# Kernel optimization log

Hardware: AMD Instinct MI355X
Metric: run time of the kernel (lower is better)

The kernel has to match this reference:

```python
import jax, jax.numpy as jnp
import numpy as np

DIM, HEADS, DH, M, PINV_ITERS, RES_K = 512, 8, 64, 256, 6, 33

def layernorm(x, w, b, eps=1e-5):
    mu = jnp.mean(x, -1, keepdims=True)
    var = jnp.var(x, -1, keepdims=True)
    return (x - mu) * jax.lax.rsqrt(var + eps) * w + b

def pinv_iter(x, iters=PINV_ITERS):
    # Moore-Penrose iterative pseudo-inverse (lucidrains nystrom-attention)
    ax = jnp.abs(x)
    z = jnp.swapaxes(x, -1, -2) / (jnp.max(ax.sum(-1)) * jnp.max(ax.sum(-2)))
    I = jnp.eye(x.shape[-1], dtype=x.dtype)
    for _ in range(iters):
        xz = x @ z
        z = 0.25 * z @ (13 * I - xz @ (15 * I - xz @ (7 * I - xz)))
    return z

def _core(x, w_qkv):
    b, n, _ = x.shape
    pad = (M - n % M) % M            # Nystrom pads at the FRONT to a multiple of m=256
    xp = jnp.pad(x, ((0, 0), (pad, 0), (0, 0)))
    npad = n + pad
    q, k, v = jnp.split(xp @ w_qkv, 3, axis=-1)
    split_heads = lambda t: t.reshape(b, npad, HEADS, DH).transpose(0, 2, 1, 3)
    q = split_heads(q) * (DH ** -0.5)
    k, v = split_heads(k), split_heads(v)
    l = npad // M                    # tokens per landmark
    q_l = q.reshape(b, HEADS, M, l, DH).mean(3)
    k_l = k.reshape(b, HEADS, M, l, DH).mean(3)
    return q, k, v, q_l, k_l, pad, n

def nystrom_out(x, w_qkv, w_out, b_out, res_kernel):
    q, k, v, q_l, k_l, pad, n = _core(x, w_qkv)
    attn1 = jax.nn.softmax(jnp.einsum('bhid,bhjd->bhij', q, k_l), -1)    # (b,h,N,M)
    attn2 = jax.nn.softmax(jnp.einsum('bhid,bhjd->bhij', q_l, k_l), -1)  # (b,h,M,M)
    attn3 = jax.nn.softmax(jnp.einsum('bhid,bhjd->bhij', q_l, k), -1)    # (b,h,M,N)
    out = (attn1 @ pinv_iter(attn2)) @ (attn3 @ v)
    # depthwise residual conv over sequence dim, per head
    out = out + jax.lax.conv_general_dilated(
        v, res_kernel, (1, 1), [(RES_K // 2, RES_K // 2), (0, 0)],
        dimension_numbers=('NCHW', 'OIHW', 'NCHW'), feature_group_count=HEADS)
    b = out.shape[0]
    out = out.transpose(0, 2, 1, 3).reshape(b, -1, HEADS * DH) @ w_out + b_out
    return out[:, -n:]

def nystrom_cls_row(x, w_qkv):
    # cls-token (query index pad, head 0) row of attn1 @ pinv(attn2) @ attn3;
    # identical math to the full (n x n) matrix row the torch code slices out.
    q, k, v, q_l, k_l, pad, n = _core(x, w_qkv)
    q0, k0, ql0, kl0 = q[:, 0], k[:, 0], q_l[:, 0], k_l[:, 0]
    attn2 = jax.nn.softmax(ql0 @ jnp.swapaxes(kl0, -1, -2), -1)   # (b,M,M)
    attn3 = jax.nn.softmax(ql0 @ jnp.swapaxes(k0, -1, -2), -1)    # (b,M,N)
    row1 = jax.nn.softmax(jnp.einsum('bd,bjd->bj', q0[:, pad], kl0), -1)
    row = jnp.einsum('bj,bjk->bk', row1, pinv_iter(attn2))
    row = jnp.einsum('bk,bkn->bn', row, attn3)                    # (b, N_padded)
    return row, pad

def dwconv(x, k, b, p):
    y = jax.lax.conv_general_dilated(x, k, (1, 1), [(p, p), (p, p)],
        dimension_numbers=('NCHW', 'OIHW', 'NCHW'), feature_group_count=x.shape[1])
    return y + b[None, :, None, None]

def leff(x, k7, b7, k5, b5, k3, b3, Hs, Ws):
    cls_t, feat = x[:, :1], x[:, 1:]
    B, N, C = feat.shape
    img = feat.transpose(0, 2, 1).reshape(B, C, Hs, Ws)
    y = dwconv(img, k7, b7, 3) + img + dwconv(img, k5, b5, 2) + dwconv(img, k3, b3, 1)
    y = y.reshape(B, C, Hs * Ws).transpose(0, 2, 1)
    return jnp.concatenate([cls_t, y], axis=1)

def setup_inputs():
    key = jax.random.key(0)
    ks = iter(jax.random.split(key, 32))
    n, n_classes = 22500, 2
    p = {}
    p['h'] = jax.random.normal(next(ks), (n, 1024), jnp.float32)
    p['fc1_w'] = jax.random.normal(next(ks), (1024, DIM), jnp.float32) * 0.02
    p['fc1_b'] = jnp.zeros((DIM,), jnp.float32)
    p['cls_token'] = jax.random.normal(next(ks), (1, 1, DIM), jnp.float32)
    for pre in ('l1', 'l2'):
        p[pre + '_ln_w'] = jnp.ones((DIM,), jnp.float32)
        p[pre + '_ln_b'] = jnp.zeros((DIM,), jnp.float32)
        p[pre + '_wqkv'] = jax.random.normal(next(ks), (DIM, 3 * HEADS * DH), jnp.float32) * 0.02
        p[pre + '_wout'] = jax.random.normal(next(ks), (HEADS * DH, DIM), jnp.float32) * 0.02
        p[pre + '_bout'] = jnp.zeros((DIM,), jnp.float32)
        p[pre + '_resk'] = jax.random.normal(next(ks), (HEADS, 1, RES_K, 1), jnp.float32) * 0.05
    for kk in (7, 5, 3):
        p['leff_k%d' % kk] = jax.random.normal(next(ks), (DIM, 1, kk, kk), jnp.float32) * 0.05
        p['leff_b%d' % kk] = jnp.zeros((DIM,), jnp.float32)
    p['norm_w'] = jnp.ones((DIM,), jnp.float32)
    p['norm_b'] = jnp.zeros((DIM,), jnp.float32)
    p['fc2_w'] = jax.random.normal(next(ks), (DIM, n_classes), jnp.float32) * 0.02
    p['fc2_b'] = jnp.zeros((n_classes,), jnp.float32)
    return p

def reference(h, fc1_w, fc1_b, cls_token,
              l1_ln_w, l1_ln_b, l1_wqkv, l1_wout, l1_bout, l1_resk,
              leff_k7, leff_b7, leff_k5, leff_b5, leff_k3, leff_b3,
              l2_ln_w, l2_ln_b, l2_wqkv, l2_wout, l2_bout, l2_resk,
              norm_w, norm_b, fc2_w, fc2_b):
    x = h[None]                                   # (1, n, 1024)
    n = x.shape[1]
    x = jax.nn.relu(x @ fc1_w + fc1_b)            # (1, n, 512)
    Hs = int(np.ceil(np.sqrt(n)))                 # 150 for n=22500
    add_len = Hs * Hs - n
    if add_len > 0:
        x = jnp.concatenate([x, x[:, :add_len]], axis=1)
    x = jnp.concatenate([jnp.broadcast_to(cls_token, (1, 1, DIM)), x], axis=1)
    # TransLayer 1
    x = x + nystrom_out(layernorm(x, l1_ln_w, l1_ln_b), l1_wqkv, l1_wout, l1_bout, l1_resk)
    # LeFF positional layer
    x = leff(x, leff_k7, leff_b7, leff_k5, leff_b5, leff_k3, leff_b3, Hs, Hs)
    # TransLayer 2 (first call in TransMIL.forward)
    h2 = x + nystrom_out(layernorm(x, l2_ln_w, l2_ln_b), l2_wqkv, l2_wout, l2_bout, l2_resk)
    # TransLayer 2 second call: residual update then attention matrix of updated state
    h3 = h2 + nystrom_out(layernorm(h2, l2_ln_w, l2_ln_b), l2_wqkv, l2_wout, l2_bout, l2_resk)
    row, pad = nystrom_cls_row(layernorm(h3, l2_ln_w, l2_ln_b), l2_wqkv)
    A = row[0, pad + 1: pad + 1 + n][:, None]     # (n, 1) cls->instance attention
    hf = layernorm(h2, norm_w, norm_b)[:, 0]      # (1, 512)
    logits = hf @ fc2_w + fc2_b                   # (1, n_classes)
    Y_prob = jax.nn.softmax(logits, -1)
    return logits, Y_prob, A
```

## Files before the change

### kernel.cpp

```cpp
#include <hip/hip_runtime.h>

#define NTOK 22500
#define N1   22501
#define NPAD 22528
#define PADR 27
#define DIM  512
#define NH   8
#define DHD  64
#define MM   256
#define LLM  88
#define HSZ  150
#define CSZ  256
#define NCH  88

typedef short bf16x8 __attribute__((ext_vector_type(8)));
typedef float f32x4  __attribute__((ext_vector_type(4)));
typedef unsigned short us;

union U8 { bf16x8 v; unsigned short u[8]; };

__device__ __forceinline__ unsigned short f2b(float f){
  unsigned int u = __float_as_uint(f);
  unsigned int r = u + 0x7fffu + ((u>>16)&1u);
  return (unsigned short)(r>>16);
}
__device__ __forceinline__ float bf2f(unsigned short u){
  return __uint_as_float(((unsigned int)u)<<16);
}
__device__ __forceinline__ bf16x8 cvt8(float4 a, float4 b){
  U8 u;
  u.u[0]=f2b(a.x); u.u[1]=f2b(a.y); u.u[2]=f2b(a.z); u.u[3]=f2b(a.w);
  u.u[4]=f2b(b.x); u.u[5]=f2b(b.y); u.u[6]=f2b(b.z); u.u[7]=f2b(b.w);
  return u.v;
}

__device__ __forceinline__ float waveSum(float v){
#pragma unroll
  for (int o=32;o>0;o>>=1) v += __shfl_down(v,o);
  return v;
}
__device__ __forceinline__ float waveMax(float v){
#pragma unroll
  for (int o=32;o>0;o>>=1) v = fmaxf(v,__shfl_down(v,o));
  return v;
}
__device__ __forceinline__ float blockSum256(float v, float* sb){
  v = waveSum(v);
  __syncthreads();
  if ((threadIdx.x&63)==0) sb[threadIdx.x>>6]=v;
  __syncthreads();
  return sb[0]+sb[1]+sb[2]+sb[3];
}
__device__ __forceinline__ float blockMax256(float v, float* sb){
  v = waveMax(v);
  __syncthreads();
  if ((threadIdx.x&63)==0) sb[threadIdx.x>>6]=v;
  __syncthreads();
  return fmaxf(fmaxf(sb[0],sb[1]),fmaxf(sb[2],sb[3]));
}

__global__ void k_wT(const float* __restrict__ W, us* __restrict__ Bt, int K, int N)
{
  __shared__ float tile[32][33];
  int tx = threadIdx.x&31, ty = threadIdx.x>>5;
  int k0 = blockIdx.x*32, n0 = blockIdx.y*32;
#pragma unroll
  for (int i=0;i<4;++i){
    int k = k0+ty+i*8;
    if (k<K && n0+tx<N) tile[ty+i*8][tx] = W[(size_t)k*N + n0+tx];
  }
  __syncthreads();
#pragma unroll
  for (int i=0;i<4;++i){
    int n = n0+ty+i*8, k = k0+tx;
    if (n<N && k<K) Bt[(size_t)n*K + k] = f2b(tile[tx][ty+i*8]);
  }
}

__global__ void k_vT(const us* __restrict__ V, us* __restrict__ Vt)
{
  __shared__ us tile[32][33];
  int tx = threadIdx.x&31, ty = threadIdx.x>>5;
  int p0 = blockIdx.x*32;
  int h = blockIdx.y>>1, d0 = (blockIdx.y&1)*32;
#pragma unroll
  for (int i=0;i<4;++i){
    int p = p0+ty+i*8;
    tile[ty+i*8][tx] = V[((size_t)h*NPAD+p)*DHD + d0+tx];
  }
  __syncthreads();
#pragma unroll
  for (int i=0;i<4;++i){
    int d = d0+ty+i*8;
    Vt[((size_t)h*DHD+d)*NPAD + p0+tx] = tile[tx][ty+i*8];
  }
}

template<int MODE>
__global__ __launch_bounds__(256) void k_gemm(const float* __restrict__ Af,
    const us* __restrict__ Ab, const us* __restrict__ Bt, const float* __restrict__ bias,
    float* __restrict__ Cf, float* __restrict__ C2,
    us* __restrict__ Q_, us* __restrict__ K_, us* __restrict__ V_, int Kd)
{
  __shared__ us SM[16384];
  us* As = SM;
  us* Bs = SM + 8192;
  const int tid = threadIdx.x;
  const int m0 = blockIdx.x*128, n0 = blockIdx.y*128;
  const int lane = tid & 63;
  const int wid = tid >> 6;
  const int wm = (wid>>1)*64, wn = (wid&1)*64;
  f32x4 acc[4][4] = {};
  for (int k0=0; k0<Kd; k0+=64){
    __syncthreads();
#pragma unroll
    for (int i=0;i<8;++i){
      int g = i*256 + tid;
      int row = g>>4, k4 = (g&15)*4;
      int gm = m0 + row;
      ushort4 h4 = make_ushort4(0,0,0,0);
      if (MODE==0){
        if (gm < NTOK){
          float4 v = *(const float4*)(Af + (size_t)gm*Kd + k0 + k4);
          h4.x=f2b(v.x); h4.y=f2b(v.y); h4.z=f2b(v.z); h4.w=f2b(v.w);
        }
      } else if (MODE==1 || MODE==3){
        if (gm >= PADR) h4 = *(const ushort4*)(Ab + (size_t)(gm-PADR)*Kd + k0 + k4);
      } else {
        if (gm < N1) h4 = *(const ushort4*)(Ab + (size_t)(gm+PADR)*Kd + k0 + k4);
      }
      *(ushort4*)(&As[row*64 + (k4 ^ ((row&7)<<3))]) = h4;
    }
#pragma unroll
    for (int i=0;i<8;++i){
      int g = i*256 + tid;
      int col = g>>4, k4 = (g&15)*4;
      int vn = n0 + col;
      if (MODE==3) vn = (vn<64) ? vn : vn+448;
      ushort4 h4 = *(const ushort4*)(Bt + (size_t)vn*Kd + k0 + k4);
      *(ushort4*)(&Bs[col*64 + (k4 ^ ((col&7)<<3))]) = h4;
    }
    __syncthreads();
#pragma unroll
    for (int ks=0; ks<2; ++ks){
      const int kk = ks*32 + (lane>>4)*8;
      bf16x8 af[4], bfm[4];
#pragma unroll
      for (int t=0;t<4;++t){
        int r = wm + t*16 + (lane&15);
        af[t] = *(bf16x8*)(&As[r*64 + (kk ^ ((r&7)<<3))]);
        int c = wn + t*16 + (lane&15);
        bfm[t] = *(bf16x8*)(&Bs[c*64 + (kk ^ ((c&7)<<3))]);
      }
#pragma unroll
      for (int mt=0;mt<4;++mt)
#pragma unroll
        for (int nt=0;nt<4;++nt)
          acc[mt][nt] = __builtin_amdgcn_mfma_f32_16x16x32_bf16(af[mt], bfm[nt], acc[mt][nt], 0,0,0);
    }
  }
  const int rbase = (lane>>4)*4;
  const int cl = lane&15;
  if (MODE==1){
    const int sec = blockIdx.y>>2;
    const float sc = sec==0 ? 0.125f : 1.f;
    __syncthreads();
#pragma unroll
    for (int mt=0;mt<4;++mt)
#pragma unroll
      for (int r=0;r<4;++r){
        int row = wm + mt*16 + rbase + r;
#pragma unroll
        for (int nt=0;nt<4;++nt){
          int col = wn + nt*16 + cl;
          SM[row*128 + col] = f2b(acc[mt][nt][r]*sc);
        }
      }
    __syncthreads();
    us* dst = sec==0 ? Q_ : (sec==1 ? K_ : V_);
#pragma unroll
    for (int i=0;i<8;++i){
      int v8 = i*256 + tid;
      int row = v8>>4, c8 = (v8&15)*8;
      int gm = m0 + row, gn = n0 + c8;
      int hh = (gn>>6)&7, d = gn&63;
      *(bf16x8*)(dst + ((size_t)hh*NPAD+gm)*DHD + d) = *(bf16x8*)(&SM[row*128 + c8]);
    }
  } else {
#pragma unroll
    for (int mt=0;mt<4;++mt){
#pragma unroll
      for (int r=0;r<4;++r){
        int gm = m0 + wm + mt*16 + rbase + r;
#pragma unroll
        for (int nt=0;nt<4;++nt){
          int gn = n0 + wn + nt*16 + cl;
          float v = acc[mt][nt][r];
          if (MODE==0){
            if (gm < NTOK){ float o = v + bias[gn]; Cf[(size_t)(1+gm)*DIM + gn] = o>0.f?o:0.f; }
          } else if (MODE==2){
            if (gm < N1) Cf[(size_t)gm*DIM + gn] += v + bias[gn];
          } else {
            if (gn < 64) Cf[(size_t)gm*DHD + gn] = v*0.125f;
            else         C2[(size_t)gm*DHD + (gn-64)] = v;
          }
        }
      }
    }
  }
}

__global__ void k_setcls(float* __restrict__ X, const float* __restrict__ cls){
  int i = blockIdx.x*256 + threadIdx.x;
  if (i < DIM) X[i] = cls[i];
}
__global__ void k_copy(float* __restrict__ d, const float* __restrict__ s, size_t n){
  size_t i = (size_t)blockIdx.x*256 + threadIdx.x;
  if (i<n) d[i]=s[i];
}

__global__ void k_ln(const float* __restrict__ X, us* __restrict__ Y,
                     const float* __restrict__ w, const float* __restrict__ b)
{
  __shared__ float sb[4];
  const float* x = X + (size_t)blockIdx.x*DIM;
  us* y = Y + (size_t)blockIdx.x*DIM;
  int t = threadIdx.x;
  float a0=x[t], a1=x[t+256];
  float s = blockSum256(a0+a1, sb);
  float q = blockSum256(a0*a0+a1*a1, sb);
  float mean = s*(1.f/512.f);
  float var = q*(1.f/512.f) - mean*mean;
  float rstd = rsqrtf(var+1e-5f);
  y[t]     = f2b((a0-mean)*rstd*w[t]+b[t]);
  y[t+256] = f2b((a1-mean)*rstd*w[t+256]+b[t+256]);
}

__global__ void k_landmark_b(const us* __restrict__ src, us* __restrict__ dst)
{
  int hm = blockIdx.x; int h = hm>>8, m = hm&255; int d = threadIdx.x;
  const us* base = src + ((size_t)h*NPAD + (size_t)m*LLM)*DHD + d;
  float s = 0.f;
  for (int j=0;j<LLM;++j) s += bf2f(base[(size_t)j*DHD]);
  dst[((size_t)h*MM + m)*DHD + d] = f2b(s * (1.f/(float)LLM));
}
__global__ void k_landmark(const float* __restrict__ src, float* __restrict__ dst)
{
  int hm = blockIdx.x; int h = hm>>8, m = hm&255; int d = threadIdx.x;
  const float* base = src + ((size_t)h*NPAD + (size_t)m*LLM)*DHD + d;
  float s = 0.f;
  for (int j=0;j<LLM;++j) s += base[(size_t)j*DHD];
  dst[((size_t)h*MM + m)*DHD + d] = s * (1.f/(float)LLM);
}

__global__ __launch_bounds__(64) void k_nt64(const float* __restrict__ A,
    const float* __restrict__ B, float* __restrict__ C,
    long sA, long sB, long sC, int Nr)
{
  int lane = threadIdx.x;
  int n0 = blockIdx.x*64, m0 = blockIdx.y*64;
  A += (size_t)blockIdx.z*sA; B += (size_t)blockIdx.z*sB; C += (size_t)blockIdx.z*sC;
  f32x4 acc[4][4] = {};
#pragma unroll
  for (int ks=0;ks<2;++ks){
    int kk = ks*32 + (lane>>4)*8;
    bf16x8 af[4], bfr[4];
#pragma unroll
    for (int mt=0;mt<4;++mt){
      const float* p = A + (size_t)(m0+mt*16+(lane&15))*64 + kk;
      af[mt] = cvt8(*(const float4*)p, *(const float4*)(p+4));
    }
#pragma unroll
    for (int nt=0;nt<4;++nt){
      const float* p = B + (size_t)(n0+nt*16+(lane&15))*64 + kk;
      bfr[nt] = cvt8(*(const float4*)p, *(const float4*)(p+4));
    }
#pragma unroll
    for (int mt=0;mt<4;++mt)
#pragma unroll
      for (int nt=0;nt<4;++nt)
        acc[mt][nt] = __builtin_amdgcn_mfma_f32_16x16x32_bf16(af[mt], bfr[nt], acc[mt][nt], 0,0,0);
  }
#pragma unroll
  for (int mt=0;mt<4;++mt)
#pragma unroll
    for (int r=0;r<4;++r){
      int row = m0+mt*16+(lane>>4)*4+r;
#pragma unroll
      for (int nt=0;nt<4;++nt){
        int col = n0+nt*16+(lane&15);
        C[(size_t)row*Nr + col] = acc[mt][nt][r];
      }
    }
}

__global__ __launch_bounds__(64) void k_nt64b(const us* __restrict__ A,
    const us* __restrict__ B, float* __restrict__ C,
    long sA, long sB, long sC, int Nr)
{
  int lane = threadIdx.x;
  int n0 = blockIdx.x*64, m0 = blockIdx.y*64;
  A += (size_t)blockIdx.z*sA; B += (size_t)blockIdx.z*sB; C += (size_t)blockIdx.z*sC;
  f32x4 acc[4][4] = {};
#pragma unroll
  for (int ks=0;ks<2;++ks){
// ... 43 lines not shown
  __syncthreads();
  const int wm = (wid>>1)*32, wn = (wid&1)*32;
  f32x4 acc[2][2] = {};
#pragma unroll
  for (int ks=0;ks<8;++ks){
    int kk = ks*32 + (lane>>4)*8;
    bf16x8 af[2], bfr[2];
#pragma unroll
    for (int t=0;t<2;++t){
      int rr = wm + t*16 + (lane&15);
      af[t] = *(const bf16x8*)(&As[rr*256 + (kk ^ ((rr&7)<<3))]);
      int cc = wn + t*16 + (lane&15);
      bfr[t] = *(const bf16x8*)(&Bs[cc*256 + (kk ^ ((cc&7)<<3))]);
    }
#pragma unroll
    for (int mt=0;mt<2;++mt)
#pragma unroll
      for (int nt=0;nt<2;++nt)
        acc[mt][nt] = __builtin_amdgcn_mfma_f32_16x16x32_bf16(af[mt], bfr[nt], acc[mt][nt], 0,0,0);
  }
#pragma unroll
  for (int mt=0;mt<2;++mt)
#pragma unroll
    for (int r=0;r<4;++r){
      int row = m0 + wm + mt*16 + (lane>>4)*4 + r;
#pragma unroll
      for (int nt=0;nt<2;++nt){
        int col = n0 + wn + nt*16 + (lane&15);
        float v = acc[mt][nt][r];
        if (PM==1) v = alpha*(dc*bf2f(Ab[(size_t)row*256+col]) - v);
        if (PM==2){
          Ct[(size_t)blockIdx.z*16384 + (size_t)col*256 + row] = f2b(v);
        } else {
          us bv = f2b(v);
          if (PM==0 || writeC) C[(size_t)blockIdx.z*65536 + (size_t)row*256 + col] = bv;
          Ct[(size_t)blockIdx.z*65536 + (size_t)col*256 + row] = bv;
        }
      }
    }
}

__global__ void k_softmax256(float* __restrict__ S, us* __restrict__ Sb)
{
  __shared__ float sb[4];
  float* row = S + ((size_t)blockIdx.x<<8);
  float x = row[threadIdx.x];
  float m = blockMax256(x, sb);
  float e = __expf(x-m);
  float s = blockSum256(e, sb);
  float p = e/s;
  row[threadIdx.x] = p;
  Sb[((size_t)blockIdx.x<<8) + threadIdx.x] = f2b(p);
}
__global__ void k_rcsum(const float* __restrict__ A2, float* __restrict__ sums, int nb)
{
  __shared__ float sb[4];
  int b = blockIdx.x >> 8, r = blockIdx.x & 255;
  const float* Ab = A2 + ((size_t)b<<16);
  float v = (blockIdx.y==0) ? Ab[((size_t)r<<8) + threadIdx.x]
                            : Ab[((size_t)threadIdx.x<<8) + r];
  float s = blockSum256(v, sb);
  if (threadIdx.x==0) sums[(size_t)blockIdx.y*nb + blockIdx.x] = s;
}
__global__ void k_scale(const float* __restrict__ sums, float* __restrict__ scl, int nb)
{
  __shared__ float sb[4];
  float mr=-1e30f, mc=-1e30f;
  for (int i=threadIdx.x;i<nb;i+=256) mr = fmaxf(mr, sums[i]);
  for (int i=threadIdx.x;i<nb;i+=256) mc = fmaxf(mc, sums[nb+i]);
  mr = blockMax256(mr, sb);
  mc = blockMax256(mc, sb);
  if (threadIdx.x==0) scl[0] = 1.f/(mr*mc);
}
__global__ void k_z0(const float* __restrict__ A2, us* __restrict__ Z, us* __restrict__ Zt,
                     const float* __restrict__ scl)
{
  size_t idx = (size_t)blockIdx.x*256 + threadIdx.x;
  size_t b = idx>>16; int i=(int)((idx>>8)&255), j=(int)(idx&255);
  float v = A2[idx]*scl[0];
  us bv = f2b(v);
  Zt[idx] = bv;
  Z[(b<<16)+((size_t)j<<8)+i] = bv;
}

__global__ __launch_bounds__(256) void k_attn3(const us* __restrict__ QLb,
    const us* __restrict__ Kb, const us* __restrict__ Vt,
    float* __restrict__ Pmax, float* __restrict__ Psum, us* __restrict__ Pacc)
{
  __shared__ us Ks[64*64];
  __shared__ us Vs[64*64];
  __shared__ us Ps[4*64*64];
  int h = blockIdx.y, cx = blockIdx.x;
  int tid = threadIdx.x, wid = tid>>6, lane = tid&63;
  bf16x8 aq[4][2];
#pragma unroll
  for (int mt=0;mt<4;++mt){
    const us* qp = QLb + ((size_t)h*MM + wid*64 + mt*16 + (lane&15))*DHD;
#pragma unroll
    for (int ks=0;ks<2;++ks)
      aq[mt][ks] = *(const bf16x8*)(qp + ks*32 + (lane>>4)*8);
  }
  float m_[4][4], l_[4][4];
  f32x4 acc[4][4] = {};
#pragma unroll
  for (int mt=0;mt<4;++mt)
#pragma unroll
    for (int r=0;r<4;++r){ m_[mt][r] = -1e30f; l_[mt][r] = 0.f; }

  us* Pw = &Ps[wid*4096];
  for (int t=0;t<4;++t){
    int kb0 = cx*CSZ + t*64;
    __syncthreads();
    for (int i=tid;i<1024;i+=256){
      int rr = i>>4, c4 = (i&15)*4;
      ushort4 ku = *(const ushort4*)(Kb + ((size_t)h*NPAD + kb0 + rr)*DHD + c4);
      *(ushort4*)(&Ks[rr*64 + (c4 ^ ((rr&7)<<3))]) = ku;
      ushort4 vu = *(const ushort4*)(Vt + ((size_t)h*DHD + rr)*NPAD + kb0 + c4);
      *(ushort4*)(&Vs[rr*64 + (c4 ^ ((rr&7)<<3))]) = vu;
    }
    __syncthreads();
    f32x4 s[4][4] = {};
#pragma unroll
    for (int ks=0;ks<2;++ks){
      int kk = ks*32 + (lane>>4)*8;
      bf16x8 kbf[4];
// ... 162 lines not shown
    int kk = ks*32 + (lane>>4)*8;
    bf16x8 a = *(const bf16x8*)(&Ps[arow*256 + (kk ^ ((arow&7)<<3))]);
#pragma unroll
    for (int dt=0;dt<4;++dt){
      int d = dt*16 + (lane&15);
      bf16x8 b = *(const bf16x8*)(&KWs[d*256 + (kk ^ ((d&7)<<3))]);
      acc[dt] = __builtin_amdgcn_mfma_f32_16x16x32_bf16(a, b, acc[dt], 0,0,0);
    }
  }
#pragma unroll
  for (int r=0;r<4;++r){
    int row = q0 + prow_base + r;
    us* op = OH + (size_t)row*DIM + h*DHD;
#pragma unroll
    for (int dt=0;dt<4;++dt)
      op[dt*16 + (lane&15)] = f2b(acc[dt][r]*rcp[r]);
  }
}

#define SCBLK 32
__global__ __launch_bounds__(256) void k_seqconv(const us* __restrict__ Vb,
    const float* __restrict__ resk, us* __restrict__ OH)
{
  __shared__ us Vs[64*512];
  int tid = threadIdx.x;
  int p0 = blockIdx.x*SCBLK;
  for (int i=tid; i<16384; i+=256){
    int pl = i>>8, c2 = i&255;
    int gp = p0 - 16 + pl;
    int hh = c2>>5, d2 = (c2&31)*2;
    ushort2 v = make_ushort2(0,0);
    if (gp>=0 && gp<NPAD) v = *(const ushort2*)(Vb + ((size_t)hh*NPAD+gp)*DHD + d2);
    *(ushort2*)(&Vs[pl*512 + c2*2]) = v;
  }
  __syncthreads();
  int h = tid>>5;
  float kr[33];
#pragma unroll
  for (int r=0;r<33;++r) kr[r] = resk[h*33+r];
  for (int pl=0; pl<SCBLK; ++pl){
    float s0=0.f, s1=0.f;
#pragma unroll
    for (int r=0;r<33;++r){
      ushort2 v = *(const ushort2*)(&Vs[(pl+r)*512 + tid*2]);
      s0 += bf2f(v.x)*kr[r];
      s1 += bf2f(v.y)*kr[r];
    }
    size_t o = (size_t)(p0+pl)*DIM + tid*2;
    ushort2 cur = *(ushort2*)(OH + o);
    *(ushort2*)(OH + o) = make_ushort2(f2b(bf2f(cur.x)+s0), f2b(bf2f(cur.y)+s1));
  }
}

__global__ void k_tfwd(const float* __restrict__ X, us* __restrict__ T)
{
  __shared__ float tile[32][33];
  int tx = threadIdx.x & 31, ty = threadIdx.x >> 5;
  int s0 = blockIdx.x*32, c0 = blockIdx.y*32;
  for (int yy=0; yy<4; ++yy){
    int s = s0 + ty + yy*8;
    if (s < NTOK) tile[ty+yy*8][tx] = X[(size_t)(1+s)*DIM + c0+tx];
  }
  __syncthreads();
  for (int yy=0; yy<4; ++yy){
    int c = c0 + ty + yy*8;
    int s = s0 + tx;
    if (s < NTOK) T[(size_t)c*NTOK + s] = f2b(tile[tx][ty+yy*8]);
  }
}
__global__ void k_tbwd(const us* __restrict__ T, float* __restrict__ X)
{
  __shared__ float tile[32][33];
  int tx = threadIdx.x & 31, ty = threadIdx.x >> 5;
  int s0 = blockIdx.x*32, c0 = blockIdx.y*32;
  for (int yy=0; yy<4; ++yy){
    int c = c0 + ty + yy*8, s = s0 + tx;
    if (s < NTOK) tile[ty+yy*8][tx] = bf2f(T[(size_t)c*NTOK + s]);
  }
  __syncthreads();
  for (int yy=0; yy<4; ++yy){
    int s = s0 + ty + yy*8, c = c0 + tx;
    if (s < NTOK) X[(size_t)(1+s)*DIM + c] = tile[tx][ty+yy*8];
  }
}
__global__ __launch_bounds__(256) void k_leff(const us* __restrict__ T,
    const float* __restrict__ k7, const float* __restrict__ b7,
    const float* __restrict__ k5, const float* __restrict__ b5,
    const float* __restrict__ k3, const float* __restrict__ b3,
    us* __restrict__ T2)
{
  __shared__ float tile[21*21];
  int c = blockIdx.y;
  int ti = blockIdx.x/10, tj = blockIdx.x%10;
  int i0 = ti*15-3, j0 = tj*15-3;
  const us* img = T + (size_t)c*NTOK;
  for (int idx=threadIdx.x; idx<441; idx+=256){
    int ii = idx/21, jj = idx%21;
    int gi = i0+ii, gj = j0+jj;
    tile[idx] = (gi>=0 && gi<HSZ && gj>=0 && gj<HSZ) ? bf2f(img[gi*HSZ+gj]) : 0.f;
  }
  __syncthreads();
  if (threadIdx.x < 225){
    int li = threadIdx.x/15, lj = threadIdx.x%15;
    int gi = ti*15+li, gj = tj*15+lj;
    float acc = tile[(li+3)*21 + (lj+3)] + b7[c]+b5[c]+b3[c];
    const float* w7 = k7 + c*49;
#pragma unroll
    for (int a=0;a<7;++a)
#pragma unroll
      for (int bb=0;bb<7;++bb) acc += tile[(li+a)*21 + (lj+bb)]*w7[a*7+bb];
    const float* w5 = k5 + c*25;
#pragma unroll
    for (int a=0;a<5;++a)
#pragma unroll
      for (int bb=0;bb<5;++bb) acc += tile[(li+1+a)*21 + (lj+1+bb)]*w5[a*5+bb];
    const float* w3 = k3 + c*9;
#pragma unroll
    for (int a=0;a<3;++a)
#pragma unroll
      for (int bb=0;bb<3;++bb) acc += tile[(li+2+a)*21 + (lj+2+bb)]*w3[a*3+bb];
    T2[(size_t)c*NTOK + gi*HSZ+gj] = f2b(acc);
  }
}

__global__ void k_row1(const float* __restrict__ Q0, const float* __restrict__ KL0,
                       float* __restrict__ row1)
{
  __shared__ float sb[4];
  __shared__ float qv[64];
  int t = threadIdx.x;
  if (t<64) qv[t] = Q0[PADR*DHD + t];
  __syncthreads();
  float l = 0.f;
#pragma unroll
  for (int d=0;d<64;++d) l += qv[d]*KL0[(size_t)t*DHD+d];
  float m = blockMax256(l, sb);
  float e = __expf(l-m);
  float s = blockSum256(e, sb);
  row1[t] = e/s;
}
__global__ void k_rz(const float* __restrict__ row1, const us* __restrict__ Zt,
                     float* __restrict__ rz)
{
  __shared__ float r1[256];
  int t = threadIdx.x;
  r1[t] = row1[t];
  __syncthreads();
  float s = 0.f;
  for (int k2=0;k2<256;++k2) s += r1[k2]*bf2f(Zt[(size_t)t*MM + k2]);
  rz[t] = s;
}
__global__ void k_rowstat(const float* __restrict__ L0, float* __restrict__ mx, float* __restrict__ se)
{
  __shared__ float sb[4];
  const float* row = L0 + (size_t)blockIdx.x*NPAD;
  float m = -1e30f;
  for (int i=threadIdx.x;i<NPAD;i+=256) m = fmaxf(m, row[i]);
  m = blockMax256(m, sb);
  float s = 0.f;
  for (int i=threadIdx.x;i<NPAD;i+=256) s += __expf(row[i]-m);
  s = blockSum256(s, sb);
  if (threadIdx.x==0){ mx[blockIdx.x]=m; se[blockIdx.x]=s; }
}
__global__ void k_aout(const float* __restrict__ L0, const float* __restrict__ rz,
    const float* __restrict__ mx, const float* __restrict__ se, float* __restrict__ out)
{
  __shared__ float wk[256], mk[256];
  int t = threadIdx.x;
  wk[t] = rz[t]/se[t];
  mk[t] = mx[t];
  __syncthreads();
  int p = blockIdx.x*256 + t;
  if (p >= NTOK) return;
  size_t pp = (size_t)(PADR+1+p);
  float a = 0.f;
  for (int k2=0;k2<256;++k2) a += wk[k2]*__expf(L0[(size_t)k2*NPAD+pp]-mk[k2]);
  out[4+p] = a;
}
__global__ void k_final(const float* __restrict__ H2r, const float* __restrict__ nw,
    const float* __restrict__ nbb, const float* __restrict__ w2, const float* __restrict__ b2,
    float* __restrict__ out)
{
  __shared__ float sb[4];
  __shared__ float hf[512];
  int t = threadIdx.x;
  float x0 = H2r[t], x1 = H2r[256+t];
  float s = blockSum256(x0+x1, sb);
  float q = blockSum256(x0*x0+x1*x1, sb);
  float mean = s*(1.f/512.f);
  float var = q*(1.f/512.f) - mean*mean;
  float rstd = rsqrtf(var+1e-5f);
  hf[t]     = (x0-mean)*rstd*nw[t]+nbb[t];
  hf[256+t] = (x1-mean)*rstd*nw[256+t]+nbb[256+t];
  __syncthreads();
  float p0 = hf[t]*w2[t*2]   + hf[256+t]*w2[(256+t)*2];
  float p1 = hf[t]*w2[t*2+1] + hf[256+t]*w2[(256+t)*2+1];
  p0 = blockSum256(p0, sb);
  p1 = blockSum256(p1, sb);
  if (t==0){
    float l0 = p0+b2[0], l1 = p1+b2[1];
    float m = fmaxf(l0,l1);
    float e0 = __expf(l0-m), e1 = __expf(l1-m), si = 1.f/(e0+e1);
    out[0]=l0; out[1]=l1; out[2]=e0*si; out[3]=e1*si;
  }
}

struct Bufs {
  float *X,*A2,*sums,*scl,*Pmax,*Psum;
  us *Yb,*OHb,*Qb,*Kb,*Vb,*Vtb,*QLb,*KLb,*A2b;
  us *Z0b,*Z0tb,*Z1b,*Z1tb,*XZb,*XZtb,*T1tb,*T2tb;
  us *A3Vtb,*WmT,*Pacc;
};

static void run_pinv(const us* A2b, Bufs& b, int NB, hipStream_t st,
                     us** outZ, us** outZt)
{
  dim3 g(4,4,NB);
  us *Zc=b.Z0b, *Zct=b.Z0tb, *Zn=b.Z1b, *Znt=b.Z1tb;
  for (int it=0; it<6; ++it){
    k_pgemm<0><<<g,256,0,st>>>(A2b, Zct, b.XZb, b.XZtb, 0.f, 1.f, 1);
    k_pgemm<1><<<g,256,0,st>>>(b.XZb, b.XZtb, nullptr, b.T1tb, 7.f, 1.f, 0);
    k_pgemm<1><<<g,256,0,st>>>(b.XZb, b.T1tb, nullptr, b.T2tb, 15.f, 1.f, 0);
    k_pgemm<1><<<g,256,0,st>>>(Zc, b.T2tb, Zn, Znt, 13.f, 0.25f, 1);
    us* t1=Zc; Zc=Zn; Zn=t1;
    us* t2=Zct; Zct=Znt; Znt=t2;
  }
  *outZ = Zc; *outZt = Zct;
}

static void nystrom_layer(Bufs& b, const float* lnw, const float* lnb,
    const us* wqkvT, const us* woutT,
    const float* bout, const float* resk, hipStream_t st)
{
  k_ln<<<N1,256,0,st>>>(b.X, b.Yb, lnw, lnb);
  k_gemm<1><<<dim3(NPAD/128,12),256,0,st>>>(nullptr, b.Yb, wqkvT, nullptr,
      nullptr, nullptr, b.Qb, b.Kb, b.Vb, DIM);
  k_vT<<<dim3(NPAD/32,16),256,0,st>>>(b.Vb, b.Vtb);
  k_landmark_b<<<NH*MM,64,0,st>>>(b.Qb, b.QLb);
  k_landmark_b<<<NH*MM,64,0,st>>>(b.Kb, b.KLb);
  k_nt64b<<<dim3(4,4,NH),64,0,st>>>(b.QLb, b.KLb, b.A2,
      (long)MM*DHD,(long)MM*DHD,(long)MM*MM, MM);
  k_softmax256<<<NH*MM,256,0,st>>>(b.A2, b.A2b);
  k_rcsum<<<dim3(NH*MM,2),256,0,st>>>(b.A2, b.sums, NH*MM);
  k_scale<<<1,256,0,st>>>(b.sums, b.scl, NH*MM);
  k_z0<<<NH*MM*MM/256,256,0,st>>>(b.A2, b.Z0b, b.Z0tb, b.scl);
  us *Zc, *Zct;
  run_pinv(b.A2b, b, NH, st, &Zc, &Zct);
  k_attn3<<<dim3(NCH,NH),256,0,st>>>(b.QLb, b.Kb, b.Vtb, b.Pmax, b.Psum, b.Pacc);
  k_attn3_merge<<<NH*MM,64,0,st>>>(b.Pmax, b.Psum, b.Pacc, b.A3Vtb);
  k_pgemm<2><<<dim3(1,4,NH),256,0,st>>>(Zc, b.A3Vtb, nullptr, b.WmT, 0.f, 1.f, 0);
  k_attn1<<<dim3(NPAD/64,NH),256,0,st>>>(b.Qb, b.KLb, b.WmT, b.OHb);
  k_seqconv<<<NPAD/SCBLK,256,0,st>>>(b.Vb, resk, b.OHb);
  k_gemm<2><<<dim3(176,4),256,0,st>>>(nullptr, b.OHb, woutT, bout,
      b.X, nullptr, nullptr, nullptr, nullptr, DIM);
}

extern "C" void kernel_launch(void* const* d_in, const int* in_sizes, int n_in,
                              void* d_out, int out_size, void* d_ws, size_t ws_size,
                              hipStream_t stream)
{
  (void)n_in; (void)out_size;
  bool sig_order = (in_sizes[10] == 25088);
  int iL2 = sig_order ? 16 : 10;
  int iLf = sig_order ? 10 : 16;

  const float* h       = (const float*)d_in[0];
  const float* fc1_w   = (const float*)d_in[1];
  const float* fc1_b   = (const float*)d_in[2];
  const float* cls_tok = (const float*)d_in[3];
  const float* l1_lnw  = (const float*)d_in[4];
  const float* l1_lnb  = (const float*)d_in[5];
  const float* l1_wqkv = (const float*)d_in[6];
  const float* l1_wout = (const float*)d_in[7];
  const float* l1_bout = (const float*)d_in[8];
  const float* l1_resk = (const float*)d_in[9];
  const float* l2_lnw  = (const float*)d_in[iL2+0];
  const float* l2_lnb  = (const float*)d_in[iL2+1];
  const float* l2_wqkv = (const float*)d_in[iL2+2];
  const float* l2_wout = (const float*)d_in[iL2+3];
  const float* l2_bout = (const float*)d_in[iL2+4];
  const float* l2_resk = (const float*)d_in[iL2+5];
  const float* k7 = (const float*)d_in[iLf+0];
  const float* b7 = (const float*)d_in[iLf+1];
  const float* k5 = (const float*)d_in[iLf+2];
  const float* b5 = (const float*)d_in[iLf+3];
  const float* k3 = (const float*)d_in[iLf+4];
  const float* b3 = (const float*)d_in[iLf+5];
  const float* nw = (const float*)d_in[22];
  const float* nbb= (const float*)d_in[23];
  const float* w2 = (const float*)d_in[24];
  const float* b2 = (const float*)d_in[25];
  float* out = (float*)d_out;

  char* base = (char*)d_ws;
  auto allocF = [&](size_t n)->float*{
    float* p=(float*)base; base += ((n*sizeof(float)+255)&~(size_t)255); return p; };
  auto allocU = [&](size_t n)->us*{
    us* p=(us*)base; base += ((n*sizeof(us)+255)&~(size_t)255); return p; };

  const size_t S = (size_t)NPAD*DIM;
  const size_t SQ = (size_t)MM*MM;
  Bufs b;
  b.X   = allocF(S);
  b.Yb  = allocU(S);
  b.OHb = allocU(S);
  b.Qb  = allocU(S);
  b.Kb  = allocU(S);
  b.Vb  = allocU(S);
  b.Vtb = allocU(S);
  b.QLb = allocU((size_t)NH*MM*DHD);
  b.KLb = allocU((size_t)NH*MM*DHD);
  b.A2  = allocF((size_t)NH*SQ);
  b.A2b = allocU((size_t)NH*SQ);
  b.Z0b = allocU((size_t)NH*SQ);  b.Z0tb = allocU((size_t)NH*SQ);
  b.Z1b = allocU((size_t)NH*SQ);  b.Z1tb = allocU((size_t)NH*SQ);
  b.XZb = allocU((size_t)NH*SQ);  b.XZtb = allocU((size_t)NH*SQ);
  b.T1tb= allocU((size_t)NH*SQ);
  b.T2tb= allocU((size_t)NH*SQ);
  b.A3Vtb = allocU((size_t)NH*MM*DHD);
  b.WmT   = allocU((size_t)NH*MM*DHD);
  b.sums  = allocF(2*(size_t)NH*MM);
  b.scl   = allocF(16);
  b.Pmax  = allocF((size_t)NH*NCH*MM);
  b.Psum  = allocF((size_t)NH*NCH*MM);
  b.Pacc  = allocU((size_t)NH*NCH*MM*DHD);
  us* fc1T   = allocU((size_t)DIM*1024);
  us* wqkvT1 = allocU((size_t)1536*DIM);
  us* wqkvT2 = allocU((size_t)1536*DIM);
  us* woutT1 = allocU((size_t)DIM*DIM);
  us* woutT2 = allocU((size_t)DIM*DIM);
  float* Q0   = allocF((size_t)NPAD*DHD);
  float* K0   = allocF((size_t)NPAD*DHD);
  float* QL0f = allocF((size_t)MM*DHD);
  float* KL0f = allocF((size_t)MM*DHD);
  float* row1 = allocF(256);
  float* rzv  = allocF(256);
  float* mxv  = allocF(256);
  float* sev  = allocF(256);
  float* h2row= allocF(512);
  if ((size_t)(base - (char*)d_ws) > ws_size) return;

  k_wT<<<dim3(32,16),256,0,stream>>>(fc1_w, fc1T, 1024, DIM);
  k_wT<<<dim3(16,48),256,0,stream>>>(l1_wqkv, wqkvT1, DIM, 1536);
  k_wT<<<dim3(16,48),256,0,stream>>>(l2_wqkv, wqkvT2, DIM, 1536);
  k_wT<<<dim3(16,16),256,0,stream>>>(l1_wout, woutT1, DIM, DIM);
  k_wT<<<dim3(16,16),256,0,stream>>>(l2_wout, woutT2, DIM, DIM);

  k_gemm<0><<<dim3(176,4),256,0,stream>>>(h, nullptr, fc1T, fc1_b,
      b.X, nullptr, nullptr, nullptr, nullptr, 1024);
  k_setcls<<<2,256,0,stream>>>(b.X, cls_tok);

  nystrom_layer(b, l1_lnw, l1_lnb, wqkvT1, woutT1, l1_bout, l1_resk, stream);
  k_tfwd<<<dim3(704,16),256,0,stream>>>(b.X, b.OHb);
  k_leff<<<dim3(100,512),256,0,stream>>>(b.OHb, k7,b7,k5,b5,k3,b3, b.Qb);
  k_tbwd<<<dim3(704,16),256,0,stream>>>(b.Qb, b.X);

  nystrom_layer(b, l2_lnw, l2_lnb, wqkvT2, woutT2, l2_bout, l2_resk, stream);
  k_copy<<<2,256,0,stream>>>(h2row, b.X, 512);

  nystrom_layer(b, l2_lnw, l2_lnb, wqkvT2, woutT2, l2_bout, l2_resk, stream);

  k_ln<<<N1,256,0,stream>>>(b.X, b.Yb, l2_lnw, l2_lnb);
  k_gemm<3><<<dim3(176,1),256,0,stream>>>(nullptr, b.Yb, wqkvT2, nullptr,
      Q0, K0, nullptr, nullptr, nullptr, DIM);
  k_landmark<<<MM,64,0,stream>>>(Q0, QL0f);
  k_landmark<<<MM,64,0,stream>>>(K0, KL0f);
  k_nt64<<<dim3(4,4,1),64,0,stream>>>(QL0f, KL0f, b.A2, 0,0,0, MM);
  k_softmax256<<<MM,256,0,stream>>>(b.A2, b.A2b);
  k_rcsum<<<dim3(MM,2),256,0,stream>>>(b.A2, b.sums, MM);
  k_scale<<<1,256,0,stream>>>(b.sums, b.scl, MM);
  k_z0<<<MM*MM/256,256,0,stream>>>(b.A2, b.Z0b, b.Z0tb, b.scl);
  us *Zc, *Zct;
  run_pinv(b.A2b, b, 1, stream, &Zc, &Zct);
  k_row1<<<1,256,0,stream>>>(Q0, KL0f, row1);
  k_rz<<<1,256,0,stream>>>(row1, Zct, rzv);
  float* L0 = (float*)b.Yb;
  k_nt64<<<dim3(NPAD/64,4,1),64,0,stream>>>(QL0f, K0, L0, 0,0,0, NPAD);
  k_rowstat<<<MM,256,0,stream>>>(L0, mxv, sev);
  k_aout<<<88,256,0,stream>>>(L0, rzv, mxv, sev, out);
  k_final<<<1,256,0,stream>>>(h2row, nw, nbb, w2, b2, out);
}
```

Measured before the change: 2.640 ms.

## Store residual stream in bf16, use direct global-to-LDS loads, merge small kernels

The residual activation buffer changes from fp32 to bf16, which halves traffic in layernorm, the output-projection residual add, the transposes and the fc1 epilogue. GEMM operand staging now uses global_load_lds 16-byte direct loads with a zero page for padded rows, and epilogues go through LDS for vectorized bf16 stores. Landmark kernels are merged, and the row/column-sum scale is replaced by a per-matrix column-sum max using the softmax row-sum-equals-one property. Rounding the residual to bf16 on every layer adds precision risk.

Result: faster. 2.487 ms (-5.8%).

```diff
diff --git a/kernel.cpp b/kernel.cpp
--- a/kernel.cpp
+++ b/kernel.cpp
@@ -33,6 +33,11 @@
   u.u[4]=f2b(b.x); u.u[5]=f2b(b.y); u.u[6]=f2b(b.z); u.u[7]=f2b(b.w);
   return u.v;
 }
+__device__ __forceinline__ void gld16(const void* g, void* l){
+  __builtin_amdgcn_global_load_lds(
+      (const __attribute__((address_space(1))) void*)g,
+      (__attribute__((address_space(3))) void*)l, 16, 0, 0);
+}
 
 __device__ __forceinline__ float waveSum(float v){
 #pragma unroll
@@ -99,8 +104,9 @@
 template<int MODE>
 __global__ __launch_bounds__(256) void k_gemm(const float* __restrict__ Af,
     const us* __restrict__ Ab, const us* __restrict__ Bt, const float* __restrict__ bias,
-    float* __restrict__ Cf, float* __restrict__ C2,
-    us* __restrict__ Q_, us* __restrict__ K_, us* __restrict__ V_, int Kd)
+    us* __restrict__ Xb, float* __restrict__ Cf, float* __restrict__ C2,
+    us* __restrict__ Q_, us* __restrict__ K_, us* __restrict__ V_,
+    const us* __restrict__ zpg, int Kd)
 {
   __shared__ us SM[16384];
   us* As = SM;
@@ -113,32 +119,40 @@
   f32x4 acc[4][4] = {};
   for (int k0=0; k0<Kd; k0+=64){
     __syncthreads();
-#pragma unroll
-    for (int i=0;i<8;++i){
-      int g = i*256 + tid;
-      int row = g>>4, k4 = (g&15)*4;
-      int gm = m0 + row;
-      ushort4 h4 = make_ushort4(0,0,0,0);
-      if (MODE==0){
+    if (MODE==0){
+#pragma unroll
+      for (int i=0;i<8;++i){
+        int g = i*256 + tid;
+        int row = g>>4, k4 = (g&15)*4;
+        int gm = m0 + row;
+        ushort4 h4 = make_ushort4(0,0,0,0);
         if (gm < NTOK){
           float4 v = *(const float4*)(Af + (size_t)gm*Kd + k0 + k4);
           h4.x=f2b(v.x); h4.y=f2b(v.y); h4.z=f2b(v.z); h4.w=f2b(v.w);
         }
-      } else if (MODE==1 || MODE==3){
-        if (gm >= PADR) h4 = *(const ushort4*)(Ab + (size_t)(gm-PADR)*Kd + k0 + k4);
-      } else {
-        if (gm < N1) h4 = *(const ushort4*)(Ab + (size_t)(gm+PADR)*Kd + k0 + k4);
-      }
-      *(ushort4*)(&As[row*64 + (k4 ^ ((row&7)<<3))]) = h4;
-    }
-#pragma unroll
-    for (int i=0;i<8;++i){
-      int g = i*256 + tid;
-      int col = g>>4, k4 = (g&15)*4;
-      int vn = n0 + col;
-      if (MODE==3) vn = (vn<64) ? vn : vn+448;
-      ushort4 h4 = *(const ushort4*)(Bt + (size_t)vn*Kd + k0 + k4);
-      *(ushort4*)(&Bs[col*64 + (k4 ^ ((col&7)<<3))]) = h4;
+        *(ushort4*)(&As[row*64 + (k4 ^ ((row&7)<<3))]) = h4;
+      }
+    } else {
+#pragma unroll
+      for (int i=0;i<4;++i){
+        int c = wid*4+i;
+        int row = c*8 + (lane>>3);
+        int scol8 = ((lane&7) ^ (row&7))*8;
+        int gm = m0+row;
+        const us* ga;
+        if (MODE==2) ga = Ab + ((size_t)((gm<N1?gm:0)+PADR))*Kd + k0 + scol8;
+        else ga = (gm>=PADR) ? Ab + (size_t)(gm-PADR)*Kd + k0 + scol8 : zpg + scol8;
+        gld16(ga, &As[c*512]);
+      }
+    }
+#pragma unroll
+    for (int i=0;i<4;++i){
+      int c = wid*4+i;
+      int row = c*8 + (lane>>3);
+      int scol8 = ((lane&7) ^ (row&7))*8;
+      int vn = n0+row;
+      if (MODE==3) vn = (vn<64)? vn : vn+448;
+      gld16(Bt + (size_t)vn*Kd + k0 + scol8, &Bs[c*512]);
     }
     __syncthreads();
 #pragma unroll
@@ -161,22 +175,42 @@
   }
   const int rbase = (lane>>4)*4;
   const int cl = lane&15;
+  if (MODE==3){
+#pragma unroll
+    for (int mt=0;mt<4;++mt)
+#pragma unroll
+      for (int r=0;r<4;++r){
+        int gm = m0 + wm + mt*16 + rbase + r;
+#pragma unroll
+        for (int nt=0;nt<4;++nt){
+          int gn = n0 + wn + nt*16 + cl;
+          float v = acc[mt][nt][r];
+          if (gn < 64) Cf[(size_t)gm*DHD + gn] = v*0.125f;
+          else         C2[(size_t)gm*DHD + (gn-64)] = v;
+        }
+      }
+    return;
+  }
+  const float sc1 = (MODE==1 && (blockIdx.y>>2)==0) ? 0.125f : 1.f;
+  __syncthreads();
+#pragma unroll
+  for (int mt=0;mt<4;++mt)
+#pragma unroll
+    for (int r=0;r<4;++r){
+      int row = wm + mt*16 + rbase + r;
+#pragma unroll
+      for (int nt=0;nt<4;++nt){
+        int col = wn + nt*16 + cl;
+        float v = acc[mt][nt][r];
+        if (MODE==0){ v += bias[n0+col]; v = v>0.f?v:0.f; }
+        else if (MODE==2){ v += bias[n0+col]; }
+        else v *= sc1;
+        SM[row*128 + col] = f2b(v);
+      }
+    }
+  __syncthreads();
   if (MODE==1){
     const int sec = blockIdx.y>>2;
-    const float sc = sec==0 ? 0.125f : 1.f;
-    __syncthreads();
-#pragma unroll
-    for (int mt=0;mt<4;++mt)
-#pragma unroll
-      for (int r=0;r<4;++r){
-        int row = wm + mt*16 + rbase + r;
-#pragma unroll
-        for (int nt=0;nt<4;++nt){
-          int col = wn + nt*16 + cl;
-          SM[row*128 + col] = f2b(acc[mt][nt][r]*sc);
-        }
-      }
-    __syncthreads();
     us* dst = sec==0 ? Q_ : (sec==1 ? K_ : V_);
 #pragma unroll
     for (int i=0;i<8;++i){
@@ -186,71 +220,87 @@
       int hh = (gn>>6)&7, d = gn&63;
       *(bf16x8*)(dst + ((size_t)hh*NPAD+gm)*DHD + d) = *(bf16x8*)(&SM[row*128 + c8]);
     }
+  } else if (MODE==0){
+#pragma unroll
+    for (int i=0;i<8;++i){
+      int v8 = i*256 + tid;
+      int row = v8>>4, c8 = (v8&15)*8;
+      int gm = m0 + row;
+      if (gm < NTOK)
+        *(bf16x8*)(Xb + (size_t)(1+gm)*DIM + n0 + c8) = *(bf16x8*)(&SM[row*128 + c8]);
+    }
   } else {
 #pragma unroll
-    for (int mt=0;mt<4;++mt){
-#pragma unroll
-      for (int r=0;r<4;++r){
-        int gm = m0 + wm + mt*16 + rbase + r;
-#pragma unroll
-        for (int nt=0;nt<4;++nt){
-          int gn = n0 + wn + nt*16 + cl;
-          float v = acc[mt][nt][r];
-          if (MODE==0){
-            if (gm < NTOK){ float o = v + bias[gn]; Cf[(size_t)(1+gm)*DIM + gn] = o>0.f?o:0.f; }
-          } else if (MODE==2){
-            if (gm < N1) Cf[(size_t)gm*DIM + gn] += v + bias[gn];
-          } else {
-            if (gn < 64) Cf[(size_t)gm*DHD + gn] = v*0.125f;
-            else         C2[(size_t)gm*DHD + (gn-64)] = v;
-          }
-        }
-      }
-    }
-  }
-}
-
-__global__ void k_setcls(float* __restrict__ X, const float* __restrict__ cls){
+    for (int i=0;i<8;++i){
+      int v8 = i*256 + tid;
+      int row = v8>>4, c8 = (v8&15)*8;
+      int gm = m0 + row;
+      if (gm < N1){
+        us* p = Xb + (size_t)gm*DIM + n0 + c8;
+        U8 xo, ad, o;
+        xo.v = *(bf16x8*)p;
+        ad.v = *(bf16x8*)(&SM[row*128 + c8]);
+#pragma unroll
+        for (int j=0;j<8;++j) o.u[j] = f2b(bf2f(xo.u[j]) + bf2f(ad.u[j]));
+        *(bf16x8*)p = o.v;
+      }
+    }
+  }
+}
+
+__global__ void k_setcls(us* __restrict__ X, const float* __restrict__ cls){
   int i = blockIdx.x*256 + threadIdx.x;
-  if (i < DIM) X[i] = cls[i];
-}
-__global__ void k_copy(float* __restrict__ d, const float* __restrict__ s, size_t n){
+  if (i < DIM) X[i] = f2b(cls[i]);
+}
+__global__ void k_copyu(us* __restrict__ d, const us* __restrict__ s, size_t n){
   size_t i = (size_t)blockIdx.x*256 + threadIdx.x;
   if (i<n) d[i]=s[i];
 }
 
-__global__ void k_ln(const float* __restrict__ X, us* __restrict__ Y,
+__global__ void k_ln(const us* __restrict__ X, us* __restrict__ Y,
                      const float* __restrict__ w, const float* __restrict__ b)
 {
   __shared__ float sb[4];
-  const float* x = X + (size_t)blockIdx.x*DIM;
+  const us* x = X + (size_t)blockIdx.x*DIM;
   us* y = Y + (size_t)blockIdx.x*DIM;
   int t = threadIdx.x;
-  float a0=x[t], a1=x[t+256];
+  ushort2 xv = *(const ushort2*)(x + 2*t);
+  float a0=bf2f(xv.x), a1=bf2f(xv.y);
   float s = blockSum256(a0+a1, sb);
   float q = blockSum256(a0*a0+a1*a1, sb);
   float mean = s*(1.f/512.f);
   float var = q*(1.f/512.f) - mean*mean;
   float rstd = rsqrtf(var+1e-5f);
-  y[t]     = f2b((a0-mean)*rstd*w[t]+b[t]);
-  y[t+256] = f2b((a1-mean)*rstd*w[t+256]+b[t+256]);
-}
-
-__global__ void k_landmark_b(const us* __restrict__ src, us* __restrict__ dst)
-{
-  int hm = blockIdx.x; int h = hm>>8, m = hm&255; int d = threadIdx.x;
-  const us* base = src + ((size_t)h*NPAD + (size_t)m*LLM)*DHD + d;
+  float2 wv = *(const float2*)(w + 2*t);
+  float2 bv = *(const float2*)(b + 2*t);
+  ushort2 o;
+  o.x = f2b((a0-mean)*rstd*wv.x+bv.x);
+  o.y = f2b((a1-mean)*rstd*wv.y+bv.y);
+  *(ushort2*)(y + 2*t) = o;
+}
+
+__global__ void k_landmark2(const us* __restrict__ Q, const us* __restrict__ K,
+                            us* __restrict__ QL, us* __restrict__ KL)
+{
+  int hm = blockIdx.x;
+  bool isK = hm >= NH*MM;
+  if (isK) hm -= NH*MM;
+  int h = hm>>8, m = hm&255; int d = threadIdx.x;
+  const us* base = (isK?K:Q) + ((size_t)h*NPAD + (size_t)m*LLM)*DHD + d;
   float s = 0.f;
   for (int j=0;j<LLM;++j) s += bf2f(base[(size_t)j*DHD]);
-  dst[((size_t)h*MM + m)*DHD + d] = f2b(s * (1.f/(float)LLM));
-}
-__global__ void k_landmark(const float* __restrict__ src, float* __restrict__ dst)
-{
-  int hm = blockIdx.x; int h = hm>>8, m = hm&255; int d = threadIdx.x;
-  const float* base = src + ((size_t)h*NPAD + (size_t)m*LLM)*DHD + d;
+  (isK?KL:QL)[((size_t)h*MM + m)*DHD + d] = f2b(s * (1.f/(float)LLM));
+}
+__global__ void k_landmark2f(const float* __restrict__ Q, const float* __restrict__ K,
+                             float* __restrict__ QL, float* __restrict__ KL)
+{
+  int hm = blockIdx.x;
+  bool isK = hm >= MM;
+  int m = isK ? hm-MM : hm; int d = threadIdx.x;
+  const float* base = (isK?K:Q) + (size_t)m*LLM*DHD + d;
   float s = 0.f;
   for (int j=0;j<LLM;++j) s += base[(size_t)j*DHD];
-  dst[((size_t)h*MM + m)*DHD + d] = s * (1.f/(float)LLM);
+  (isK?KL:QL)[(size_t)m*DHD + d] = s * (1.f/(float)LLM);
 }
 
 __global__ __launch_bounds__(64) void k_nt64(const float* __restrict__ A,
@@ -400,25 +450,23 @@
   row[threadIdx.x] = p;
   Sb[((size_t)blockIdx.x<<8) + threadIdx.x] = f2b(p);
 }
-__global__ void k_rcsum(const float* __restrict__ A2, float* __restrict__ sums, int nb)
+__global__ void k_csmax(const float* __restrict__ A2, float* __restrict__ sums)
 {
   __shared__ float sb[4];
-  int b = blockIdx.x >> 8, r = blockIdx.x & 255;
+  int b = blockIdx.x, j = threadIdx.x;
   const float* Ab = A2 + ((size_t)b<<16);
-  float v = (blockIdx.y==0) ? Ab[((size_t)r<<8) + threadIdx.x]
-                            : Ab[((size_t)threadIdx.x<<8) + r];
-  float s = blockSum256(v, sb);
-  if (threadIdx.x==0) sums[(size_t)blockIdx.y*nb + blockIdx.x] = s;
-}
-__global__ void k_scale(const float* __restrict__ sums, float* __restrict__ scl, int nb)
+  float s = 0.f;
+  for (int i=0;i<256;++i) s += Ab[((size_t)i<<8)+j];
+  float m = blockMax256(s, sb);
+  if (j==0) sums[b] = m;
+}
+__global__ void k_scale2(const float* __restrict__ sums, float* __restrict__ scl, int nb)
 {
   __shared__ float sb[4];
-  float mr=-1e30f, mc=-1e30f;
-  for (int i=threadIdx.x;i<nb;i+=256) mr = fmaxf(mr, sums[i]);
-  for (int i=threadIdx.x;i<nb;i+=256) mc = fmaxf(mc, sums[nb+i]);
-  mr = blockMax256(mr, sb);
-  mc = blockMax256(mc, sb);
-  if (threadIdx.x==0) scl[0] = 1.f/(mr*mc);
+  float m=-1e30f;
+  for (int i=threadIdx.x;i<nb;i+=256) m = fmaxf(m, sums[i]);
+  m = blockMax256(m, sb);
+  if (threadIdx.x==0) scl[0] = 1.f/m;
 }
 __global__ void k_z0(const float* __restrict__ A2, us* __restrict__ Z, us* __restrict__ Zt,
                      const float* __restrict__ scl)
@@ -687,9 +735,9 @@
   }
 }
 
-__global__ void k_tfwd(const float* __restrict__ X, us* __restrict__ T)
-{
-  __shared__ float tile[32][33];
+__global__ void k_tfwd(const us* __restrict__ X, us* __restrict__ T)
+{
+  __shared__ us tile[32][33];
   int tx = threadIdx.x & 31, ty = threadIdx.x >> 5;
   int s0 = blockIdx.x*32, c0 = blockIdx.y*32;
   for (int yy=0; yy<4; ++yy){
@@ -700,17 +748,17 @@
   for (int yy=0; yy<4; ++yy){
     int c = c0 + ty + yy*8;
     int s = s0 + tx;
-    if (s < NTOK) T[(size_t)c*NTOK + s] = f2b(tile[tx][ty+yy*8]);
-  }
-}
-__global__ void k_tbwd(const us* __restrict__ T, float* __restrict__ X)
-{
-  __shared__ float tile[32][33];
+    if (s < NTOK) T[(size_t)c*NTOK + s] = tile[tx][ty+yy*8];
+  }
+}
+__global__ void k_tbwd(const us* __restrict__ T, us* __restrict__ X)
+{
+  __shared__ us tile[32][33];
   int tx = threadIdx.x & 31, ty = threadIdx.x >> 5;
   int s0 = blockIdx.x*32, c0 = blockIdx.y*32;
   for (int yy=0; yy<4; ++yy){
     int c = c0 + ty + yy*8, s = s0 + tx;
-    if (s < NTOK) tile[ty+yy*8][tx] = bf2f(T[(size_t)c*NTOK + s]);
+    if (s < NTOK) tile[ty+yy*8][tx] = T[(size_t)c*NTOK + s];
   }
   __syncthreads();
   for (int yy=0; yy<4; ++yy){
@@ -812,14 +860,14 @@
   for (int k2=0;k2<256;++k2) a += wk[k2]*__expf(L0[(size_t)k2*NPAD+pp]-mk[k2]);
   out[4+p] = a;
 }
-__global__ void k_final(const float* __restrict__ H2r, const float* __restrict__ nw,
+__global__ void k_final(const us* __restrict__ H2r, const float* __restrict__ nw,
     const float* __restrict__ nbb, const float* __restrict__ w2, const float* __restrict__ b2,
     float* __restrict__ out)
 {
   __shared__ float sb[4];
   __shared__ float hf[512];
   int t = threadIdx.x;
-  float x0 = H2r[t], x1 = H2r[256+t];
+  float x0 = bf2f(H2r[t]), x1 = bf2f(H2r[256+t]);
   float s = blockSum256(x0+x1, sb);
   float q = blockSum256(x0*x0+x1*x1, sb);
   float mean = s*(1.f/512.f);
@@ -841,10 +889,10 @@
 }
 
 struct Bufs {
-  float *X,*A2,*sums,*scl,*Pmax,*Psum;
-  us *Yb,*OHb,*Qb,*Kb,*Vb,*Vtb,*QLb,*KLb,*A2b;
+  float *A2,*sums,*scl,*Pmax,*Psum;
+  us *Xb,*Yb,*OHb,*Qb,*Kb,*Vb,*Vtb,*QLb,*KLb,*A2b;
   us *Z0b,*Z0tb,*Z1b,*Z1tb,*XZb,*XZtb,*T1tb,*T2tb;
-  us *A3Vtb,*WmT,*Pacc;
+  us *A3Vtb,*WmT,*Pacc,*zpg;
 };
 
 static void run_pinv(const us* A2b, Bufs& b, int NB, hipStream_t st,
@@ -867,17 +915,16 @@
     const us* wqkvT, const us* woutT,
     const float* bout, const float* resk, hipStream_t st)
 {
-  k_ln<<<N1,256,0,st>>>(b.X, b.Yb, lnw, lnb);
+  k_ln<<<N1,256,0,st>>>(b.Xb, b.Yb, lnw, lnb);
   k_gemm<1><<<dim3(NPAD/128,12),256,0,st>>>(nullptr, b.Yb, wqkvT, nullptr,
-      nullptr, nullptr, b.Qb, b.Kb, b.Vb, DIM);
+      nullptr, nullptr, nullptr, b.Qb, b.Kb, b.Vb, b.zpg, DIM);
   k_vT<<<dim3(NPAD/32,16),256,0,st>>>(b.Vb, b.Vtb);
-  k_landmark_b<<<NH*MM,64,0,st>>>(b.Qb, b.QLb);
-  k_landmark_b<<<NH*MM,64,0,st>>>(b.Kb, b.KLb);
+  k_landmark2<<<2*NH*MM,64,0,st>>>(b.Qb, b.Kb, b.QLb, b.KLb);
   k_nt64b<<<dim3(4,4,NH),64,0,st>>>(b.QLb, b.KLb, b.A2,
       (long)MM*DHD,(long)MM*DHD,(long)MM*MM, MM);
   k_softmax256<<<NH*MM,256,0,st>>>(b.A2, b.A2b);
-  k_rcsum<<<dim3(NH*MM,2),256,0,st>>>(b.A2, b.sums, NH*MM);
-  k_scale<<<1,256,0,st>>>(b.sums, b.scl, NH*MM);
+  k_csmax<<<NH,256,0,st>>>(b.A2, b.sums);
+  k_scale2<<<1,256,0,st>>>(b.sums, b.scl, NH);
   k_z0<<<NH*MM*MM/256,256,0,st>>>(b.A2, b.Z0b, b.Z0tb, b.scl);
   us *Zc, *Zct;
   run_pinv(b.A2b, b, NH, st, &Zc, &Zct);
@@ -887,7 +934,7 @@
   k_attn1<<<dim3(NPAD/64,NH),256,0,st>>>(b.Qb, b.KLb, b.WmT, b.OHb);
   k_seqconv<<<NPAD/SCBLK,256,0,st>>>(b.Vb, resk, b.OHb);
   k_gemm<2><<<dim3(176,4),256,0,st>>>(nullptr, b.OHb, woutT, bout,
-      b.X, nullptr, nullptr, nullptr, nullptr, DIM);
+      b.Xb, nullptr, nullptr, nullptr, nullptr, nullptr, b.zpg, DIM);
 }
 
 extern "C" void kernel_launch(void* const* d_in, const int* in_sizes, int n_in,
@@ -936,7 +983,7 @@
   const size_t S = (size_t)NPAD*DIM;
   const size_t SQ = (size_t)MM*MM;
   Bufs b;
-  b.X   = allocF(S);
+  b.Xb  = allocU(S);
   b.Yb  = allocU(S);
   b.OHb = allocU(S);
   b.Qb  = allocU(S);
@@ -959,6 +1006,7 @@
   b.Pmax  = allocF((size_t)NH*NCH*MM);
   b.Psum  = allocF((size_t)NH*NCH*MM);
   b.Pacc  = allocU((size_t)NH*NCH*MM*DHD);
+  b.zpg   = allocU(512);
   us* fc1T   = allocU((size_t)DIM*1024);
   us* wqkvT1 = allocU((size_t)1536*DIM);
   us* wqkvT2 = allocU((size_t)1536*DIM);
@@ -972,8 +1020,10 @@
   float* rzv  = allocF(256);
   float* mxv  = allocF(256);
   float* sev  = allocF(256);
-  float* h2row= allocF(512);
+  us* h2row = allocU(512);
   if ((size_t)(base - (char*)d_ws) > ws_size) return;
+
+  hipMemsetAsync((void*)b.zpg, 0, 1024, stream);
 
   k_wT<<<dim3(32,16),256,0,stream>>>(fc1_w, fc1T, 1024, DIM);
   k_wT<<<dim3(16,48),256,0,stream>>>(l1_wqkv, wqkvT1, DIM, 1536);
@@ -982,28 +1032,27 @@
   k_wT<<<dim3(16,16),256,0,stream>>>(l2_wout, woutT2, DIM, DIM);
 
   k_gemm<0><<<dim3(176,4),256,0,stream>>>(h, nullptr, fc1T, fc1_b,
-      b.X, nullptr, nullptr, nullptr, nullptr, 1024);
-  k_setcls<<<2,256,0,stream>>>(b.X, cls_tok);
+      b.Xb, nullptr, nullptr, nullptr, nullptr, nullptr, b.zpg, 1024);
+  k_setcls<<<2,256,0,stream>>>(b.Xb, cls_tok);
 
   nystrom_layer(b, l1_lnw, l1_lnb, wqkvT1, woutT1, l1_bout, l1_resk, stream);
-  k_tfwd<<<dim3(704,16),256,0,stream>>>(b.X, b.OHb);
+  k_tfwd<<<dim3(704,16),256,0,stream>>>(b.Xb, b.OHb);
   k_leff<<<dim3(100,512),256,0,stream>>>(b.OHb, k7,b7,k5,b5,k3,b3, b.Qb);
-  k_tbwd<<<dim3(704,16),256,0,stream>>>(b.Qb, b.X);
+  k_tbwd<<<dim3(704,16),256,0,stream>>>(b.Qb, b.Xb);
 
   nystrom_layer(b, l2_lnw, l2_lnb, wqkvT2, woutT2, l2_bout, l2_resk, stream);
-  k_copy<<<2,256,0,stream>>>(h2row, b.X, 512);
+  k_copyu<<<2,256,0,stream>>>(h2row, b.Xb, 512);
 
   nystrom_layer(b, l2_lnw, l2_lnb, wqkvT2, woutT2, l2_bout, l2_resk, stream);
 
-  k_ln<<<N1,256,0,stream>>>(b.X, b.Yb, l2_lnw, l2_lnb);
+  k_ln<<<N1,256,0,stream>>>(b.Xb, b.Yb, l2_lnw, l2_lnb);
   k_gemm<3><<<dim3(176,1),256,0,stream>>>(nullptr, b.Yb, wqkvT2, nullptr,
-      Q0, K0, nullptr, nullptr, nullptr, DIM);
-  k_landmark<<<MM,64,0,stream>>>(Q0, QL0f);
-  k_landmark<<<MM,64,0,stream>>>(K0, KL0f);
+      nullptr, Q0, K0, nullptr, nullptr, nullptr, b.zpg, DIM);
+  k_landmark2f<<<2*MM,64,0,stream>>>(Q0, K0, QL0f, KL0f);
   k_nt64<<<dim3(4,4,1),64,0,stream>>>(QL0f, KL0f, b.A2, 0,0,0, MM);
   k_softmax256<<<MM,256,0,stream>>>(b.A2, b.A2b);
-  k_rcsum<<<dim3(MM,2),256,0,stream>>>(b.A2, b.sums, MM);
-  k_scale<<<1,256,0,stream>>>(b.sums, b.scl, MM);
+  k_csmax<<<1,256,0,stream>>>(b.A2, b.sums);
+  k_scale2<<<1,256,0,stream>>>(b.sums, b.scl, 1);
   k_z0<<<MM*MM/256,256,0,stream>>>(b.A2, b.Z0b, b.Z0tb, b.scl);
   us *Zc, *Zct;
   run_pinv(b.A2b, b, 1, stream, &Zc, &Zct);
```
